# Optimization experiments

Measured on AMD Instinct MI355X. Metric: run time of the kernel, lower is better.

The kernel has to match this reference:

```python
import jax, jax.numpy as jnp
import numpy as np

B, P, C, O = 64, 8732, 81, 16
THRESH = 0.5
NEGPOS = 3
VAR0, VAR1 = 0.1, 0.2


def setup_inputs() -> dict:
    key = jax.random.key(0)
    k1, k2, k3, k4, k5, k6, k7 = jax.random.split(key, 7)
    # ground-truth boxes in point form (xmin,ymin,xmax,ymax), valid and inside [0,1]
    lo = jax.random.uniform(k1, (B, O, 2), minval=0.0, maxval=0.7)
    wh = jax.random.uniform(k2, (B, O, 2), minval=0.05, maxval=0.3)
    truths = jnp.concatenate([lo, lo + wh], axis=-1)
    labels = jax.random.randint(k3, (B, O), 0, C - 1).astype(jnp.int32)
    # prior boxes in center-size form with strictly positive w/h
    ctr = jax.random.uniform(k4, (P, 2), minval=0.05, maxval=0.95)
    pwh = jax.random.uniform(k5, (P, 2), minval=0.05, maxval=0.5)
    dbox = jnp.concatenate([ctr, pwh], axis=-1)
    loc_data = jax.random.normal(k6, (B, P, 4), dtype=jnp.float32)
    conf_data = jax.random.normal(k7, (B, P, C), dtype=jnp.float32)
    return {"loc_data": loc_data, "conf_data": conf_data, "dbox": dbox,
            "truths": truths, "labels": labels}


def point_form(boxes):
    return jnp.concatenate([boxes[:, :2] - boxes[:, 2:] / 2,
                            boxes[:, :2] + boxes[:, 2:] / 2], axis=1)


def jaccard(box_a, box_b):
    # box_a: [A,4], box_b: [B,4] point form -> IoU [A,B]
    max_xy = jnp.minimum(box_a[:, None, 2:], box_b[None, :, 2:])
    min_xy = jnp.maximum(box_a[:, None, :2], box_b[None, :, :2])
    inter = jnp.prod(jnp.clip(max_xy - min_xy, 0.0, None), axis=-1)  # [A,B]
    area_a = jnp.prod(box_a[:, 2:] - box_a[:, :2], axis=-1)[:, None]
    area_b = jnp.prod(box_b[:, 2:] - box_b[:, :2], axis=-1)[None, :]
    return inter / (area_a + area_b - inter)


def encode(matched, priors):
    g_cxcy = ((matched[:, :2] + matched[:, 2:]) / 2 - priors[:, :2]) / (VAR0 * priors[:, 2:])
    g_wh = jnp.log((matched[:, 2:] - matched[:, :2]) / priors[:, 2:]) / VAR1
    return jnp.concatenate([g_cxcy, g_wh], axis=1)


def match_one(truths, labels, priors, priors_pf):
    overlaps = jaccard(truths, priors_pf)                  # [O, P]
    best_prior_idx = jnp.argmax(overlaps, axis=1)          # [O]
    best_truth_overlap = jnp.max(overlaps, axis=0)         # [P]
    best_truth_idx = jnp.argmax(overlaps, axis=0)          # [P]
    best_truth_overlap = best_truth_overlap.at[best_prior_idx].set(2.0)
    best_truth_idx = best_truth_idx.at[best_prior_idx].set(jnp.arange(truths.shape[0]))
    matches = truths[best_truth_idx]                       # [P,4]
    conf = jnp.where(best_truth_overlap < THRESH, 0, labels[best_truth_idx] + 1)
    loc = encode(matches, priors)                          # [P,4]
    return loc, conf


def reference(loc_data, conf_data, dbox, truths, labels):
    priors_pf = point_form(dbox)
    loc_t, conf_t = jax.vmap(match_one, in_axes=(0, 0, None, None))(
        truths, labels, dbox, priors_pf)                   # [B,P,4], [B,P]

    pos_mask = conf_t > 0                                  # [B,P]
    # localization smooth-L1 (beta=1) over positive priors
    d = jnp.abs(loc_data - loc_t)
    sl1 = jnp.where(d < 1.0, 0.5 * d * d, d - 0.5)
    loss_l = jnp.sum(sl1 * pos_mask[..., None].astype(sl1.dtype))

    # per-prior cross entropy
    logz = jax.nn.logsumexp(conf_data, axis=-1)            # [B,P]
    picked = jnp.take_along_axis(conf_data, conf_t[..., None], axis=-1)[..., 0]
    ce = logz - picked                                     # [B,P]

    # hard negative mining: rank negatives by CE (positives zeroed)
    loss_c_neg = jnp.where(pos_mask, 0.0, ce)
    order = jnp.argsort(-loss_c_neg, axis=1)
    idx_rank = jnp.argsort(order, axis=1)
    num_pos = jnp.sum(pos_mask, axis=1, keepdims=True)     # [B,1]
    num_neg = jnp.clip(num_pos * NEGPOS, None, P)
    neg_mask = idx_rank < num_neg

    sel = (pos_mask | neg_mask).astype(ce.dtype)
    loss_c = jnp.sum(ce * sel)

    N = jnp.sum(num_pos).astype(loss_l.dtype)
    return loss_l / N, loss_c / N
```

## Files before the change

### kernel.cpp

```cpp
#include <hip/hip_runtime.h>
#include <stdint.h>
#include <math.h>

#define B 64
#define P 8732
#define C 81
#define O 16
#define THRESH 0.5f
#define NEGPOS 3
#define VAR0 0.1f
#define VAR1 0.2f

#define ITER 4
#define ROWS_PER_WAVE (8 * ITER)
#define ROWS_PER_BLOCK (4 * ROWS_PER_WAVE)

__global__ __launch_bounds__(1024) void bp_k(const float* __restrict__ dbox,
                                             const float* __restrict__ truths,
                                             int* __restrict__ forced_p,
                                             int* __restrict__ num_pos,
                                             float* __restrict__ possum,
                                             float* __restrict__ lossl,
                                             float* __restrict__ acc,
                                             int* __restrict__ done) {
    const int b = blockIdx.x;
    const int tid = threadIdx.x;
    if (b == 0) {
        if (tid < B) { num_pos[tid] = 0; possum[tid] = 0.f; lossl[tid] = 0.f; }
        if (tid == B) { acc[0] = 0.f; acc[1] = 0.f; }
        if (tid == B + 1) { *done = 0; }
    }
    const int lane = tid & 63;
    const int o = tid >> 6;
    const float tx0 = truths[(b * O + o) * 4 + 0];
    const float ty0 = truths[(b * O + o) * 4 + 1];
    const float tx1 = truths[(b * O + o) * 4 + 2];
    const float ty1 = truths[(b * O + o) * 4 + 3];
    const float ta = (tx1 - tx0) * (ty1 - ty0);

    unsigned long long best = 0ull;
    for (int p = lane; p < P; p += 64) {
        const float4 db = *(const float4*)(dbox + (size_t)p * 4);
        const float px0 = db.x - db.z * 0.5f, py0 = db.y - db.w * 0.5f;
        const float px1 = db.x + db.z * 0.5f, py1 = db.y + db.w * 0.5f;
        const float parea = (px1 - px0) * (py1 - py0);
        float ix = fminf(tx1, px1) - fmaxf(tx0, px0);
        float iy = fminf(ty1, py1) - fmaxf(ty0, py0);
        ix = fmaxf(ix, 0.f); iy = fmaxf(iy, 0.f);
        const float inter = ix * iy;
        const float ov = inter / (ta + parea - inter);
        const unsigned long long key =
            ((unsigned long long)__float_as_uint(ov) << 32) |
            (unsigned long long)(0xFFFFFFFFu - (unsigned)p);
        if (key > best) best = key;
    }
    for (int off = 32; off; off >>= 1) {
        const unsigned long long o2 = __shfl_xor(best, off);
        if (o2 > best) best = o2;
    }
    if (lane == 0)
        forced_p[b * O + o] = (int)(0xFFFFFFFFu - (unsigned)(best & 0xFFFFFFFFull));
}

__global__ __launch_bounds__(256) void loss_k(
        const float* __restrict__ loc_data,
        const float* __restrict__ conf_data,
        const float* __restrict__ dbox,
        const float* __restrict__ truths,
        const int* __restrict__ labels,
        const int* __restrict__ forced_p,
        float* __restrict__ negce,
        int* __restrict__ num_pos, float* __restrict__ possum,
        float* __restrict__ lossl) {
    const int b = blockIdx.y;
    const int tid = threadIdx.x;
    const int lane = tid & 63;
    const int wid = tid >> 6;
    const int sub = lane & 15;
    const int g = lane >> 4;

    __shared__ float s_truth[O * 4];
    __shared__ int s_fp[O];
    __shared__ int s_lab[O];
    __shared__ float s_l, s_p;
    __shared__ int s_n;
    if (tid < O * 4) s_truth[tid] = truths[b * O * 4 + tid];
    if (tid < O) { s_fp[tid] = forced_p[b * O + tid]; s_lab[tid] = labels[b * O + tid]; }
    if (tid == 0) { s_l = 0.f; s_p = 0.f; s_n = 0; }
    __syncthreads();

    const float tx0 = s_truth[sub * 4 + 0], ty0 = s_truth[sub * 4 + 1];
    const float tx1 = s_truth[sub * 4 + 2], ty1 = s_truth[sub * 4 + 3];
    const float tarea = (tx1 - tx0) * (ty1 - ty0);

    float l_acc = 0.f;
    float p_acc = 0.f;
    int n_acc = 0;

    const int wbase = blockIdx.x * ROWS_PER_BLOCK + wid * ROWS_PER_WAVE;

    for (int r = 0; r < ITER; ++r) {
        const int pA = wbase + 8 * r + g;
        const int pB = pA + 4;
        const bool actA = (pA < P), actB = (pB < P);
        const size_t rowA = (size_t)b * P + (actA ? pA : P - 1);
        const size_t rowB = (size_t)b * P + (actB ? pB : P - 1);

        const float* rpA = conf_data + rowA * C;
        const float* rpB = conf_data + rowB * C;
        float vA[5], vB[5];
#pragma unroll
        for (int j = 0; j < 5; ++j) vA[j] = rpA[sub + 16 * j];
#pragma unroll
        for (int j = 0; j < 5; ++j) vB[j] = rpB[sub + 16 * j];
        const float vA80 = rpA[80];
        const float vB80 = rpB[80];
        const float4 dbA = *(const float4*)(dbox + rowA % P * 4);
        const float4 dbB = *(const float4*)(dbox + rowB % P * 4);

        float ovA, ovB;
        int tiA = sub, tiB = sub;
        {
            const float pax0 = dbA.x - dbA.z * 0.5f, pay0 = dbA.y - dbA.w * 0.5f;
            const float pax1 = dbA.x + dbA.z * 0.5f, pay1 = dbA.y + dbA.w * 0.5f;
            const float pareaA = (pax1 - pax0) * (pay1 - pay0);
            float ixA = fminf(tx1, pax1) - fmaxf(tx0, pax0);
            float iyA = fminf(ty1, pay1) - fmaxf(ty0, pay0);
            ixA = fmaxf(ixA, 0.f); iyA = fmaxf(iyA, 0.f);
            const float interA = ixA * iyA;
            ovA = interA / (tarea + pareaA - interA);

            const float pbx0 = dbB.x - dbB.z * 0.5f, pby0 = dbB.y - dbB.w * 0.5f;
            const float pbx1 = dbB.x + dbB.z * 0.5f, pby1 = dbB.y + dbB.w * 0.5f;
            const float pareaB = (pbx1 - pbx0) * (pby1 - pby0);
            float ixB = fminf(tx1, pbx1) - fmaxf(tx0, pbx0);
            float iyB = fminf(ty1, pby1) - fmaxf(ty0, pby0);
            ixB = fmaxf(ixB, 0.f); iyB = fmaxf(iyB, 0.f);
            const float interB = ixB * iyB;
            ovB = interB / (tarea + pareaB - interB);
        }
        for (int off = 8; off; off >>= 1) {
            const float oA = __shfl_xor(ovA, off);
            const int iA = __shfl_xor(tiA, off);
            const float oB = __shfl_xor(ovB, off);
            const int iB = __shfl_xor(tiB, off);
            if (oA > ovA || (oA == ovA && iA < tiA)) { ovA = oA; tiA = iA; }
            if (oB > ovB || (oB == ovB && iB < tiB)) { ovB = oB; tiB = iB; }
        }
        bool fA = false, fB = false;
#pragma unroll
        for (int o = 0; o < O; ++o) {
            if (s_fp[o] == pA) { tiA = o; fA = true; }
            if (s_fp[o] == pB) { tiB = o; fB = true; }
        }
        const int confA = (fA || ovA >= THRESH) ? (s_lab[tiA] + 1) : 0;
        const int confB = (fB || ovB >= THRESH) ? (s_lab[tiB] + 1) : 0;
        const bool posA = confA > 0, posB = confB > 0;

        float sA = 0.f, pkA = 0.f, sB = 0.f, pkB = 0.f;
#pragma unroll
        for (int j = 0; j < 5; ++j) {
            sA += __expf(vA[j]);
            sB += __expf(vB[j]);
            pkA += (sub + 16 * j == confA) ? vA[j] : 0.f;
            pkB += (sub + 16 * j == confB) ? vB[j] : 0.f;
        }
        if (sub == 0) {
            sA += __expf(vA80);
            sB += __expf(vB80);
            if (confA == 80) pkA = vA80;
            if (confB == 80) pkB = vB80;
        }
        for (int off = 8; off; off >>= 1) {
            sA += __shfl_xor(sA, off);
            sB += __shfl_xor(sB, off);
            pkA += __shfl_xor(pkA, off);
            pkB += __shfl_xor(pkB, off);
        }
        const float cevA = __logf(sA) - pkA;
        const float cevB = __logf(sB) - pkB;

        if (actA && sub == 0) {
            negce[rowA] = posA ? 0.f : cevA;
            if (posA) { p_acc += cevA; n_acc++; }
        }
        if (actB && sub == 0) {
            negce[rowB] = posB ? 0.f : cevB;
            if (posB) { p_acc += cevB; n_acc++; }
        }
        if (actA && posA && sub < 4) {
            const float mx0 = s_truth[tiA * 4 + 0], my0 = s_truth[tiA * 4 + 1];
            const float mx1 = s_truth[tiA * 4 + 2], my1 = s_truth[tiA * 4 + 3];
            float tgt;
            if (sub == 0)      tgt = ((mx0 + mx1) * 0.5f - dbA.x) / (VAR0 * dbA.z);
            else if (sub == 1) tgt = ((my0 + my1) * 0.5f - dbA.y) / (VAR0 * dbA.w);
            else if (sub == 2) tgt = logf((mx1 - mx0) / dbA.z) / VAR1;
            else               tgt = logf((my1 - my0) / dbA.w) / VAR1;
            const float d = fabsf(loc_data[rowA * 4 + sub] - tgt);
            l_acc += (d < 1.f) ? 0.5f * d * d : d - 0.5f;
        }
        if (actB && posB && sub < 4) {
            const float mx0 = s_truth[tiB * 4 + 0], my0 = s_truth[tiB * 4 + 1];
            const float mx1 = s_truth[tiB * 4 + 2], my1 = s_truth[tiB * 4 + 3];
            float tgt;
            if (sub == 0)      tgt = ((mx0 + mx1) * 0.5f - dbB.x) / (VAR0 * dbB.z);
            else if (sub == 1) tgt = ((my0 + my1) * 0.5f - dbB.y) / (VAR0 * dbB.w);
            else if (sub == 2) tgt = logf((mx1 - mx0) / dbB.z) / VAR1;
            else               tgt = logf((my1 - my0) / dbB.w) / VAR1;
            const float d = fabsf(loc_data[rowB * 4 + sub] - tgt);
            l_acc += (d < 1.f) ? 0.5f * d * d : d - 0.5f;
        }
    }
    for (int off = 32; off; off >>= 1) {
        l_acc += __shfl_xor(l_acc, off);
        p_acc += __shfl_xor(p_acc, off);
        n_acc += __shfl_xor(n_acc, off);
    }
    if (lane == 0) {
        atomicAdd(&s_l, l_acc);
        atomicAdd(&s_p, p_acc);
        atomicAdd(&s_n, n_acc);
    }
    __syncthreads();
    if (tid == 0) {
        atomicAdd(&lossl[b], s_l);
        atomicAdd(&possum[b], s_p);
        atomicAdd(&num_pos[b], s_n);
    }
}

__global__ __launch_bounds__(1024) void mine_k(
        const float* __restrict__ negce,
        const int* __restrict__ num_pos,
        const float* __restrict__ possum,
        const float* __restrict__ lossl,
        float* __restrict__ acc, int* __restrict__ done,
        float* __restrict__ out) {
    const int b = blockIdx.x;
    const int tid = threadIdx.x;
    const int lane = tid & 63;
    const int wid = tid >> 6;
    const float* x = negce + (size_t)b * P;
    float v[9];
#pragma unroll
    for (int j = 0; j < 9; ++j) {
        const int i = tid + j * 1024;
        v[j] = (i < P) ? x[i] : -1.0f;
    }
    int k = num_pos[b] * NEGPOS;
    if (k > P) k = P;

    __shared__ int wred[2][16];
    __shared__ float wsumf[16];
    __shared__ int wcnt[16];
    float S = 0.f;
    if (k > 0) {
        unsigned lo = 0u, hi = 0x7F800000u;
        int parity = 0;
        while (lo < hi) {
            const unsigned mid = lo + ((hi - lo) >> 1);
            const float t = __uint_as_float(mid);
            int cnt = 0;
#pragma unroll
            for (int j = 0; j < 9; ++j) cnt += (v[j] > t) ? 1 : 0;
            for (int off = 32; off; off >>= 1) cnt += __shfl_xor(cnt, off);
            if (lane == 0) wred[parity][wid] = cnt;
            __syncthreads();
            int total = 0;
#pragma unroll
            for (int w = 0; w < 16; ++w) total += wred[parity][w];
            if (total < k) hi = mid; else lo = mid + 1;
            parity ^= 1;
        }
        const float t = __uint_as_float(lo);
        float sum = 0.f;
        int cnt = 0;
#pragma unroll
        for (int j = 0; j < 9; ++j) {
            if (v[j] > t) { sum += v[j]; cnt++; }
        }
        for (int off = 32; off; off >>= 1) {
            sum += __shfl_xor(sum, off);
            cnt += __shfl_xor(cnt, off);
        }
        if (lane == 0) { wsumf[wid] = sum; wcnt[wid] = cnt; }
        __syncthreads();
        if (tid == 0) {
            float ts = 0.f; int tc = 0;
#pragma unroll
            for (int w = 0; w < 16; ++w) { ts += wsumf[w]; tc += wcnt[w]; }
            S = ts + (float)(k - tc) * t;
        }
    }
    if (tid == 0) {
        atomicAdd(&acc[1], possum[b] + S);
        __threadfence();
        const int prev = atomicAdd(done, 1);
        if (prev == B - 1) {
            __threadfence();
            float N = 0.f, L = 0.f;
            for (int i = 0; i < B; ++i) { N += (float)num_pos[i]; L += lossl[i]; }
            const float cval = atomicAdd(&acc[1], 0.0f);
            out[0] = L / N;
            out[1] = cval / N;
        }
    }
}

extern "C" void kernel_launch(void* const* d_in, const int* in_sizes, int n_in,
                              void* d_out, int out_size, void* d_ws, size_t ws_size,
                              hipStream_t stream) {
    (void)in_sizes; (void)n_in; (void)out_size; (void)ws_size;
    const float* loc_data  = (const float*)d_in[0];
    const float* conf_data = (const float*)d_in[1];
    const float* dbox      = (const float*)d_in[2];
    const float* truths    = (const float*)d_in[3];
    const int*   labels    = (const int*)d_in[4];
    float* out = (float*)d_out;

    int* forced_p = (int*)d_ws;
    float* negce  = (float*)(forced_p + B * O);
    int* num_pos  = (int*)(negce + (size_t)B * P);
    float* possum = (float*)(num_pos + B);
    float* lossl  = possum + B;
    float* acc    = lossl + B;
    int* done     = (int*)(acc + 2);

    bp_k<<<B, 1024, 0, stream>>>(dbox, truths, forced_p,
                                 num_pos, possum, lossl, acc, done);
    loss_k<<<dim3((P + ROWS_PER_BLOCK - 1) / ROWS_PER_BLOCK, B), 256, 0, stream>>>(
        loc_data, conf_data, dbox, truths, labels, forced_p,
        negce, num_pos, possum, lossl);
    mine_k<<<B, 1024, 0, stream>>>(negce, num_pos, possum, lossl, acc, done, out);
}
```

Baseline: 367.7 us.

## Vectorize conf loads, use ballot/shuffle for matching, split best-prior kernel into more blocks

The best-prior kernel launches 256 smaller blocks of 256 threads instead of 64 blocks of 1024, and unrolls its prior loop by four. In the loss kernel, each lane now loads a contiguous float4 of confidence logits plus one scalar instead of five strided scalars. The shared-memory scan over forced-prior indices is replaced by a wave ballot, and label lookup uses a shuffle. The picked logit is taken with a single shuffle instead of a masked sum reduction, which drops one reduction chain and the shared-memory reads.

```diff
diff --git a/kernel.cpp b/kernel.cpp
--- a/kernel.cpp
+++ b/kernel.cpp
@@ -15,44 +15,47 @@
 #define ROWS_PER_WAVE (8 * ITER)
 #define ROWS_PER_BLOCK (4 * ROWS_PER_WAVE)
 
-__global__ __launch_bounds__(1024) void bp_k(const float* __restrict__ dbox,
-                                             const float* __restrict__ truths,
-                                             int* __restrict__ forced_p,
-                                             int* __restrict__ num_pos,
-                                             float* __restrict__ possum,
-                                             float* __restrict__ lossl,
-                                             float* __restrict__ acc,
-                                             int* __restrict__ done) {
-    const int b = blockIdx.x;
+__global__ __launch_bounds__(256) void bp_k(const float* __restrict__ dbox,
+                                            const float* __restrict__ truths,
+                                            int* __restrict__ forced_p,
+                                            int* __restrict__ num_pos,
+                                            float* __restrict__ possum,
+                                            float* __restrict__ lossl,
+                                            float* __restrict__ acc,
+                                            int* __restrict__ done) {
     const int tid = threadIdx.x;
-    if (b == 0) {
+    if (blockIdx.x == 0) {
         if (tid < B) { num_pos[tid] = 0; possum[tid] = 0.f; lossl[tid] = 0.f; }
         if (tid == B) { acc[0] = 0.f; acc[1] = 0.f; }
         if (tid == B + 1) { *done = 0; }
     }
     const int lane = tid & 63;
-    const int o = tid >> 6;
-    const float tx0 = truths[(b * O + o) * 4 + 0];
-    const float ty0 = truths[(b * O + o) * 4 + 1];
-    const float tx1 = truths[(b * O + o) * 4 + 2];
-    const float ty1 = truths[(b * O + o) * 4 + 3];
-    const float ta = (tx1 - tx0) * (ty1 - ty0);
+    const int gw = blockIdx.x * 4 + (tid >> 6);
+    const int b = gw >> 4, o = gw & 15;
+    const float4 t = *(const float4*)(truths + (size_t)(b * O + o) * 4);
+    const float ta = (t.z - t.x) * (t.w - t.y);
 
     unsigned long long best = 0ull;
-    for (int p = lane; p < P; p += 64) {
-        const float4 db = *(const float4*)(dbox + (size_t)p * 4);
-        const float px0 = db.x - db.z * 0.5f, py0 = db.y - db.w * 0.5f;
-        const float px1 = db.x + db.z * 0.5f, py1 = db.y + db.w * 0.5f;
-        const float parea = (px1 - px0) * (py1 - py0);
-        float ix = fminf(tx1, px1) - fmaxf(tx0, px0);
-        float iy = fminf(ty1, py1) - fmaxf(ty0, py0);
-        ix = fmaxf(ix, 0.f); iy = fmaxf(iy, 0.f);
-        const float inter = ix * iy;
-        const float ov = inter / (ta + parea - inter);
-        const unsigned long long key =
-            ((unsigned long long)__float_as_uint(ov) << 32) |
-            (unsigned long long)(0xFFFFFFFFu - (unsigned)p);
-        if (key > best) best = key;
+    for (int p0 = lane; p0 < P; p0 += 256) {
+#pragma unroll
+        for (int u = 0; u < 4; ++u) {
+            const int p = p0 + 64 * u;
+            if (p < P) {
+                const float4 db = *(const float4*)(dbox + (size_t)p * 4);
+                const float px0 = db.x - db.z * 0.5f, py0 = db.y - db.w * 0.5f;
+                const float px1 = db.x + db.z * 0.5f, py1 = db.y + db.w * 0.5f;
+                const float parea = (px1 - px0) * (py1 - py0);
+                float ix = fminf(t.z, px1) - fmaxf(t.x, px0);
+                float iy = fminf(t.w, py1) - fmaxf(t.y, py0);
+                ix = fmaxf(ix, 0.f); iy = fmaxf(iy, 0.f);
+                const float inter = ix * iy;
+                const float ov = inter / (ta + parea - inter);
+                const unsigned long long key =
+                    ((unsigned long long)__float_as_uint(ov) << 32) |
+                    (unsigned long long)(0xFFFFFFFFu - (unsigned)p);
+                if (key > best) best = key;
+            }
+        }
     }
     for (int off = 32; off; off >>= 1) {
         const unsigned long long o2 = __shfl_xor(best, off);
@@ -77,21 +80,19 @@
     const int lane = tid & 63;
     const int wid = tid >> 6;
     const int sub = lane & 15;
-    const int g = lane >> 4;
+    const int gbase = lane & 48;
 
     __shared__ float s_truth[O * 4];
-    __shared__ int s_fp[O];
-    __shared__ int s_lab[O];
     __shared__ float s_l, s_p;
     __shared__ int s_n;
     if (tid < O * 4) s_truth[tid] = truths[b * O * 4 + tid];
-    if (tid < O) { s_fp[tid] = forced_p[b * O + tid]; s_lab[tid] = labels[b * O + tid]; }
     if (tid == 0) { s_l = 0.f; s_p = 0.f; s_n = 0; }
+
+    const float4 tt = *(const float4*)(truths + (size_t)(b * O + sub) * 4);
+    const int f_reg = forced_p[b * O + sub];
+    const int lab_reg = labels[b * O + sub];
+    const float tarea = (tt.z - tt.x) * (tt.w - tt.y);
     __syncthreads();
-
-    const float tx0 = s_truth[sub * 4 + 0], ty0 = s_truth[sub * 4 + 1];
-    const float tx1 = s_truth[sub * 4 + 2], ty1 = s_truth[sub * 4 + 3];
-    const float tarea = (tx1 - tx0) * (ty1 - ty0);
 
     float l_acc = 0.f;
     float p_acc = 0.f;
@@ -100,23 +101,24 @@
     const int wbase = blockIdx.x * ROWS_PER_BLOCK + wid * ROWS_PER_WAVE;
 
     for (int r = 0; r < ITER; ++r) {
-        const int pA = wbase + 8 * r + g;
+        const int pA = wbase + 8 * r + (gbase >> 4);
         const int pB = pA + 4;
         const bool actA = (pA < P), actB = (pB < P);
-        const size_t rowA = (size_t)b * P + (actA ? pA : P - 1);
-        const size_t rowB = (size_t)b * P + (actB ? pB : P - 1);
+        const int dA = actA ? pA : P - 1;
+        const int dB = actB ? pB : P - 1;
+        const size_t rowA = (size_t)b * P + dA;
+        const size_t rowB = (size_t)b * P + dB;
 
         const float* rpA = conf_data + rowA * C;
         const float* rpB = conf_data + rowB * C;
-        float vA[5], vB[5];
-#pragma unroll
-        for (int j = 0; j < 5; ++j) vA[j] = rpA[sub + 16 * j];
-#pragma unroll
-        for (int j = 0; j < 5; ++j) vB[j] = rpB[sub + 16 * j];
-        const float vA80 = rpA[80];
-        const float vB80 = rpB[80];
-        const float4 dbA = *(const float4*)(dbox + rowA % P * 4);
-        const float4 dbB = *(const float4*)(dbox + rowB % P * 4);
+        const float4 qA = *(const float4*)(rpA + 4 * sub);
+        const float4 qB = *(const float4*)(rpB + 4 * sub);
+        const float eA = rpA[64 + sub];
+        const float eB = rpB[64 + sub];
+        const float e80A = rpA[80];
+        const float e80B = rpB[80];
+        const float4 dbA = *(const float4*)(dbox + (size_t)dA * 4);
+        const float4 dbB = *(const float4*)(dbox + (size_t)dB * 4);
 
         float ovA, ovB;
         int tiA = sub, tiB = sub;
@@ -124,8 +126,8 @@
             const float pax0 = dbA.x - dbA.z * 0.5f, pay0 = dbA.y - dbA.w * 0.5f;
             const float pax1 = dbA.x + dbA.z * 0.5f, pay1 = dbA.y + dbA.w * 0.5f;
             const float pareaA = (pax1 - pax0) * (pay1 - pay0);
-            float ixA = fminf(tx1, pax1) - fmaxf(tx0, pax0);
-            float iyA = fminf(ty1, pay1) - fmaxf(ty0, pay0);
+            float ixA = fminf(tt.z, pax1) - fmaxf(tt.x, pax0);
+            float iyA = fminf(tt.w, pay1) - fmaxf(tt.y, pay0);
             ixA = fmaxf(ixA, 0.f); iyA = fmaxf(iyA, 0.f);
             const float interA = ixA * iyA;
             ovA = interA / (tarea + pareaA - interA);
@@ -133,8 +135,8 @@
             const float pbx0 = dbB.x - dbB.z * 0.5f, pby0 = dbB.y - dbB.w * 0.5f;
             const float pbx1 = dbB.x + dbB.z * 0.5f, pby1 = dbB.y + dbB.w * 0.5f;
             const float pareaB = (pbx1 - pbx0) * (pby1 - pby0);
-            float ixB = fminf(tx1, pbx1) - fmaxf(tx0, pbx0);
-            float iyB = fminf(ty1, pby1) - fmaxf(ty0, pby0);
+            float ixB = fminf(tt.z, pbx1) - fmaxf(tt.x, pbx0);
+            float iyB = fminf(tt.w, pby1) - fmaxf(tt.y, pby0);
             ixB = fmaxf(ixB, 0.f); iyB = fmaxf(iyB, 0.f);
             const float interB = ixB * iyB;
             ovB = interB / (tarea + pareaB - interB);
@@ -147,36 +149,41 @@
             if (oA > ovA || (oA == ovA && iA < tiA)) { ovA = oA; tiA = iA; }
             if (oB > ovB || (oB == ovB && iB < tiB)) { ovB = oB; tiB = iB; }
         }
-        bool fA = false, fB = false;
-#pragma unroll
-        for (int o = 0; o < O; ++o) {
-            if (s_fp[o] == pA) { tiA = o; fA = true; }
-            if (s_fp[o] == pB) { tiB = o; fB = true; }
-        }
-        const int confA = (fA || ovA >= THRESH) ? (s_lab[tiA] + 1) : 0;
-        const int confB = (fB || ovB >= THRESH) ? (s_lab[tiB] + 1) : 0;
+        const unsigned long long balA = __ballot(f_reg == pA);
+        const unsigned long long balB = __ballot(f_reg == pB);
+        const unsigned mA = (unsigned)(balA >> gbase) & 0xFFFFu;
+        const unsigned mB = (unsigned)(balB >> gbase) & 0xFFFFu;
+        const bool fA = (mA != 0), fB = (mB != 0);
+        if (fA) tiA = 31 - __clz(mA);
+        if (fB) tiB = 31 - __clz(mB);
+        const int labA = __shfl(lab_reg, gbase | tiA);
+        const int labB = __shfl(lab_reg, gbase | tiB);
+        const int confA = (fA || ovA >= THRESH) ? (labA + 1) : 0;
+        const int confB = (fB || ovB >= THRESH) ? (labB + 1) : 0;
         const bool posA = confA > 0, posB = confB > 0;
 
-        float sA = 0.f, pkA = 0.f, sB = 0.f, pkB = 0.f;
-#pragma unroll
-        for (int j = 0; j < 5; ++j) {
-            sA += __expf(vA[j]);
-            sB += __expf(vB[j]);
-            pkA += (sub + 16 * j == confA) ? vA[j] : 0.f;
-            pkB += (sub + 16 * j == confB) ? vB[j] : 0.f;
-        }
-        if (sub == 0) {
-            sA += __expf(vA80);
-            sB += __expf(vB80);
-            if (confA == 80) pkA = vA80;
-            if (confB == 80) pkB = vB80;
-        }
+        float sA = __expf(qA.x) + __expf(qA.y) + __expf(qA.z) + __expf(qA.w) + __expf(eA);
+        float sB = __expf(qB.x) + __expf(qB.y) + __expf(qB.z) + __expf(qB.w) + __expf(eB);
         for (int off = 8; off; off >>= 1) {
             sA += __shfl_xor(sA, off);
             sB += __shfl_xor(sB, off);
-            pkA += __shfl_xor(pkA, off);
-            pkB += __shfl_xor(pkB, off);
-        }
+        }
+        sA += __expf(e80A);
+        sB += __expf(e80B);
+
+        const float selA = (confA < 64)
+            ? ((confA & 2) ? ((confA & 1) ? qA.w : qA.z) : ((confA & 1) ? qA.y : qA.x))
+            : eA;
+        const float selB = (confB < 64)
+            ? ((confB & 2) ? ((confB & 1) ? qB.w : qB.z) : ((confB & 1) ? qB.y : qB.x))
+            : eB;
+        const int hA = (confA < 64) ? (confA >> 2) : (confA & 15);
+        const int hB = (confB < 64) ? (confB >> 2) : (confB & 15);
+        float pkA = __shfl(selA, gbase | hA);
+        float pkB = __shfl(selB, gbase | hB);
+        if (confA == 80) pkA = e80A;
+        if (confB == 80) pkB = e80B;
+
         const float cevA = __logf(sA) - pkA;
         const float cevB = __logf(sB) - pkB;
 
@@ -326,8 +333,8 @@
     float* acc    = lossl + B;
     int* done     = (int*)(acc + 2);
 
-    bp_k<<<B, 1024, 0, stream>>>(dbox, truths, forced_p,
-                                 num_pos, possum, lossl, acc, done);
+    bp_k<<<(B * O) / 4, 256, 0, stream>>>(dbox, truths, forced_p,
+                                          num_pos, possum, lossl, acc, done);
     loss_k<<<dim3((P + ROWS_PER_BLOCK - 1) / ROWS_PER_BLOCK, B), 256, 0, stream>>>(
         loc_data, conf_data, dbox, truths, labels, forced_p,
         negce, num_pos, possum, lossl);
```

Measured after the change: 367.3 us. About the same (-0.1%).
